# Performance work log

Hardware: AMD Instinct MI355X
Metric: run time of the kernel (lower is better)

## Reference

```python
import jax, jax.numpy as jnp
import numpy as np

B, D, NQ, NS = 64, 64, 2048, 2048

def setup_inputs() -> dict:
    key = jax.random.key(0)
    k1, k2 = jax.random.split(key)
    query_local = jax.random.normal(k1, (B, D, NQ), dtype=jnp.float32)
    support_local = jax.random.normal(k2, (B, D, NS), dtype=jnp.float32)
    return {"query_local": query_local, "support_local": support_local}

def reference(query_local, support_local):
    # sim[b, q, s] = sum_d query[b, d, q] * support[b, d, s]  -> (B, N_q, N_s)
    sim = jnp.einsum('bdq,bds->bqs', query_local, support_local)
    best_sim = jnp.max(sim, axis=2)        # (B, N_q)
    return jnp.mean(best_sim, axis=1)      # (B,)
```

## Files before the change

### kernel.cpp

```cpp
#include <hip/hip_runtime.h>
#include <hip/hip_bf16.h>

#define NB 64
#define ND 64
#define NQ 2048
#define NS 2048
#define QBLK 512
#define SBLK 64
#define QPB 4
#define NSPLIT 2
#define NSS (NS / NSPLIT)
#define NT (NSS / SBLK)

typedef float f32x4 __attribute__((ext_vector_type(4)));
typedef short bf16x8 __attribute__((ext_vector_type(8)));
typedef int i32x4 __attribute__((ext_vector_type(4)));

__device__ inline i32x4 pack8(const float* f) {
  union { __hip_bfloat162 h2[4]; i32x4 v; } u;
  #pragma unroll
  for (int p = 0; p < 4; ++p)
    u.h2[p] = __float22bfloat162_rn(float2{f[2 * p], f[2 * p + 1]});
  return u.v;
}

#define BAR() asm volatile("s_waitcnt lgkmcnt(0)\n\ts_barrier" ::: "memory")

__global__ __launch_bounds__(512, 2) void bmd_main(
    const float* __restrict__ Q, const float* __restrict__ S,
    float* __restrict__ part) {
  const int bid = blockIdx.x;
  const int b  = bid & (NB - 1);
  const int qb = (bid >> 6) & (QPB - 1);
  const int ss = bid >> 8;
  const int q0 = qb * QBLK;
  const int sbase = ss * NSS;
  const int tid = threadIdx.x;
  const int lane = tid & 63;
  const int w = tid >> 6;

  __shared__ char sT[2][SBLK * 128];

  const float* Qb = Q + (size_t)b * ND * NQ;
  const float* Sb = S + (size_t)b * ND * NS;

  const int dbq = (tid >> 3) & 7;
  const int sl = (tid & 7) + ((tid >> 6) << 3);
  const int byt = sl * 128 + ((dbq ^ (sl & 7)) << 4);
  const float* stage_src = Sb + (size_t)dbq * 8 * NS + sbase;

  float fA[8], fB[8];
  {
    const float* s0 = stage_src + sl;
    #pragma unroll
    for (int e = 0; e < 8; ++e) fA[e] = s0[(size_t)e * NS];
    const float* s1 = stage_src + SBLK + sl;
    #pragma unroll
    for (int e = 0; e < 8; ++e) fB[e] = s1[(size_t)e * NS];
  }

  i32x4 afrag[4][2];
  {
    const int qrow = q0 + w * 64 + (lane & 15);
    const int dbase = (lane >> 4) * 8;
    for (int mf = 0; mf < 4; ++mf)
      for (int ks = 0; ks < 2; ++ks) {
        const int d0 = ks * 32 + dbase;
        float f[8];
        #pragma unroll
        for (int e = 0; e < 8; ++e)
          f[e] = Qb[(size_t)(d0 + e) * NQ + (qrow + mf * 16)];
        afrag[mf][ks] = pack8(f);
      }
  }

  const f32x4 kZero = {0.f, 0.f, 0.f, 0.f};
  f32x4 rmax[4];
  #pragma unroll
  for (int mf = 0; mf < 4; ++mf)
    rmax[mf] = f32x4{-INFINITY, -INFINITY, -INFINITY, -INFINITY};

#define COMPUTE(buf)                                                          \
  {                                                                           \
    __builtin_amdgcn_s_setprio(1);                                            \
    _Pragma("unroll")                                                         \
    for (int nfp = 0; nfp < 2; ++nfp) {                                       \
      const int scol0 = nfp * 32 + (lane & 15);                               \
      bf16x8 bfr0[2], bfr1[2];                                                \
      _Pragma("unroll")                                                       \
      for (int ks = 0; ks < 2; ++ks) {                                        \
        const int slot = ((ks * 4 + (lane >> 4)) ^ (scol0 & 7)) << 4;         \
        bfr0[ks] = *reinterpret_cast<const bf16x8*>((buf) + scol0 * 128 + slot);        \
        bfr1[ks] = *reinterpret_cast<const bf16x8*>((buf) + (scol0 + 16) * 128 + slot); \
      }                                                                       \
      _Pragma("unroll")                                                       \
      for (int mf = 0; mf < 4; ++mf) {                                        \
        const bf16x8 a0 = __builtin_bit_cast(bf16x8, afrag[mf][0]);           \
        const bf16x8 a1 = __builtin_bit_cast(bf16x8, afrag[mf][1]);           \
        f32x4 acc0 = __builtin_amdgcn_mfma_f32_16x16x32_bf16(a0, bfr0[0], kZero, 0, 0, 0); \
        f32x4 acc1 = __builtin_amdgcn_mfma_f32_16x16x32_bf16(a0, bfr1[0], kZero, 0, 0, 0); \
        acc0 = __builtin_amdgcn_mfma_f32_16x16x32_bf16(a1, bfr0[1], acc0, 0, 0, 0);        \
        acc1 = __builtin_amdgcn_mfma_f32_16x16x32_bf16(a1, bfr1[1], acc1, 0, 0, 0);        \
        _Pragma("unroll")                                                     \
        for (int j = 0; j < 4; ++j)                                           \
          rmax[mf][j] = fmaxf(rmax[mf][j], fmaxf(acc0[j], acc1[j]));          \
      }                                                                       \
    }                                                                         \
    __builtin_amdgcn_s_setprio(0);                                            \
  }

  *reinterpret_cast<i32x4*>(sT[0] + byt) = pack8(fA);
  BAR();

  for (int i = 0; i < NT / 2; ++i) {
    const int t = 2 * i;
    if (t + 2 < NT) {
      const float* src = stage_src + (t + 2) * SBLK + sl;
      #pragma unroll
      for (int e = 0; e < 8; ++e) fA[e] = src[(size_t)e * NS];
    }
    *reinterpret_cast<i32x4*>(sT[1] + byt) = pack8(fB);
    COMPUTE(sT[0]);
    BAR();
    if (t + 3 < NT) {
      const float* src = stage_src + (t + 3) * SBLK + sl;
      #pragma unroll
      for (int e = 0; e < 8; ++e) fB[e] = src[(size_t)e * NS];
    }
    if (t + 2 < NT)
      *reinterpret_cast<i32x4*>(sT[0] + byt) = pack8(fA);
    COMPUTE(sT[1]);
    BAR();
  }
#undef COMPUTE

  float* rowp = part + (size_t)bid * QBLK + w * 64;
  #pragma unroll
  for (int mf = 0; mf < 4; ++mf) {
    #pragma unroll
    for (int j = 0; j < 4; ++j) {
      float v = rmax[mf][j];
      v = fmaxf(v, __shfl_xor(v, 1));
      v = fmaxf(v, __shfl_xor(v, 2));
      v = fmaxf(v, __shfl_xor(v, 4));
      v = fmaxf(v, __shfl_xor(v, 8));
      if ((lane & 15) == 0)
        rowp[mf * 16 + (lane >> 4) * 4 + j] = v;
    }
  }
}

__global__ void bmd_reduce(const float* __restrict__ part, float* __restrict__ out) {
  const int b = blockIdx.x;
  const int tid = threadIdx.x;
  __shared__ float ws4[4];
  float sum = 0.f;
  #pragma unroll
  for (int k = 0; k < NQ / 256; ++k) {
    const int q = k * 256 + tid;
    const int qb = q >> 9;
    const int row = q & (QBLK - 1);
    float m = -INFINITY;
    #pragma unroll
    for (int ssi = 0; ssi < NSPLIT; ++ssi)
      m = fmaxf(m, part[((size_t)((ssi * QPB + qb) * NB + b)) * QBLK + row]);
    sum += m;
  }
  #pragma unroll
  for (int o = 1; o < 64; o <<= 1) sum += __shfl_xor(sum, o);
  if ((tid & 63) == 0) ws4[tid >> 6] = sum;
  __syncthreads();
  if (tid == 0) out[b] = (ws4[0] + ws4[1] + ws4[2] + ws4[3]) * (1.0f / NQ);
}

extern "C" void kernel_launch(void* const* d_in, const int* in_sizes, int n_in,
                              void* d_out, int out_size, void* d_ws, size_t ws_size,
                              hipStream_t stream) {
  const float* Q = (const float*)d_in[0];
  const float* S = (const float*)d_in[1];
  float* out = (float*)d_out;
  float* part = (float*)d_ws;
  bmd_main<<<dim3(NB * QPB * NSPLIT), dim3(512), 0, stream>>>(Q, S, part);
  bmd_reduce<<<dim3(NB), dim3(256), 0, stream>>>(part, out);
}
```

Before: 51.54 us.

## Split tile compute into barrier-separated phases interleaving LDS loads, staging and MFMA

Each 64-column tile computation is split into two half-phases. Every phase issues its LDS fragment reads first, then the global load or LDS store for the next tile, then a barrier before the MFMA block. The aim is to spread global and LDS traffic across the whole iteration and overlap it with matrix work across waves, similar to a ping-pong schedule. In exchange the loop runs about four times as many s_barrier instructions, which adds synchronization stalls. Correctness depends on waitcnt placement relative to those barriers.

```diff
diff --git a/kernel.cpp b/kernel.cpp
--- a/kernel.cpp
+++ b/kernel.cpp
@@ -24,8 +24,6 @@
   return u.v;
 }
 
-#define BAR() asm volatile("s_waitcnt lgkmcnt(0)\n\ts_barrier" ::: "memory")
-
 __global__ __launch_bounds__(512, 2) void bmd_main(
     const float* __restrict__ Q, const float* __restrict__ S,
     float* __restrict__ part) {
@@ -40,6 +38,8 @@
   const int w = tid >> 6;
 
   __shared__ char sT[2][SBLK * 128];
+  char* const sT0p = sT[0];
+  char* const sT1p = sT[1];
 
   const float* Qb = Q + (size_t)b * ND * NQ;
   const float* Sb = S + (size_t)b * ND * NS;
@@ -80,59 +80,64 @@
   for (int mf = 0; mf < 4; ++mf)
     rmax[mf] = f32x4{-INFINITY, -INFINITY, -INFINITY, -INFINITY};
 
-#define COMPUTE(buf)                                                          \
+#define PHASE(bufptr, nfp, STAGE_CODE)                                        \
   {                                                                           \
+    const int scol0 = (nfp) * 32 + (lane & 15);                               \
+    bf16x8 bfr0[2], bfr1[2];                                                  \
+    _Pragma("unroll")                                                         \
+    for (int ks = 0; ks < 2; ++ks) {                                          \
+      const int slot = ((ks * 4 + (lane >> 4)) ^ (scol0 & 7)) << 4;           \
+      bfr0[ks] = *reinterpret_cast<const bf16x8*>((bufptr) + scol0 * 128 + slot);        \
+      bfr1[ks] = *reinterpret_cast<const bf16x8*>((bufptr) + (scol0 + 16) * 128 + slot); \
+    }                                                                         \
+    STAGE_CODE;                                                               \
+    asm volatile("s_barrier" ::: "memory");                                   \
+    asm volatile("s_waitcnt lgkmcnt(0)" ::: "memory");                        \
     __builtin_amdgcn_s_setprio(1);                                            \
     _Pragma("unroll")                                                         \
-    for (int nfp = 0; nfp < 2; ++nfp) {                                       \
-      const int scol0 = nfp * 32 + (lane & 15);                               \
-      bf16x8 bfr0[2], bfr1[2];                                                \
+    for (int mf = 0; mf < 4; ++mf) {                                          \
+      const bf16x8 a0 = __builtin_bit_cast(bf16x8, afrag[mf][0]);             \
+      const bf16x8 a1 = __builtin_bit_cast(bf16x8, afrag[mf][1]);             \
+      f32x4 acc0 = __builtin_amdgcn_mfma_f32_16x16x32_bf16(a0, bfr0[0], kZero, 0, 0, 0); \
+      f32x4 acc1 = __builtin_amdgcn_mfma_f32_16x16x32_bf16(a0, bfr1[0], kZero, 0, 0, 0); \
+      acc0 = __builtin_amdgcn_mfma_f32_16x16x32_bf16(a1, bfr0[1], acc0, 0, 0, 0);        \
+      acc1 = __builtin_amdgcn_mfma_f32_16x16x32_bf16(a1, bfr1[1], acc1, 0, 0, 0);        \
       _Pragma("unroll")                                                       \
-      for (int ks = 0; ks < 2; ++ks) {                                        \
-        const int slot = ((ks * 4 + (lane >> 4)) ^ (scol0 & 7)) << 4;         \
-        bfr0[ks] = *reinterpret_cast<const bf16x8*>((buf) + scol0 * 128 + slot);        \
-        bfr1[ks] = *reinterpret_cast<const bf16x8*>((buf) + (scol0 + 16) * 128 + slot); \
-      }                                                                       \
-      _Pragma("unroll")                                                       \
-      for (int mf = 0; mf < 4; ++mf) {                                        \
-        const bf16x8 a0 = __builtin_bit_cast(bf16x8, afrag[mf][0]);           \
-        const bf16x8 a1 = __builtin_bit_cast(bf16x8, afrag[mf][1]);           \
-        f32x4 acc0 = __builtin_amdgcn_mfma_f32_16x16x32_bf16(a0, bfr0[0], kZero, 0, 0, 0); \
-        f32x4 acc1 = __builtin_amdgcn_mfma_f32_16x16x32_bf16(a0, bfr1[0], kZero, 0, 0, 0); \
-        acc0 = __builtin_amdgcn_mfma_f32_16x16x32_bf16(a1, bfr0[1], acc0, 0, 0, 0);        \
-        acc1 = __builtin_amdgcn_mfma_f32_16x16x32_bf16(a1, bfr1[1], acc1, 0, 0, 0);        \
-        _Pragma("unroll")                                                     \
-        for (int j = 0; j < 4; ++j)                                           \
-          rmax[mf][j] = fmaxf(rmax[mf][j], fmaxf(acc0[j], acc1[j]));          \
-      }                                                                       \
+      for (int j = 0; j < 4; ++j)                                             \
+        rmax[mf][j] = fmaxf(rmax[mf][j], fmaxf(acc0[j], acc1[j]));            \
     }                                                                         \
     __builtin_amdgcn_s_setprio(0);                                            \
+    asm volatile("s_barrier" ::: "memory");                                   \
   }
 
-  *reinterpret_cast<i32x4*>(sT[0] + byt) = pack8(fA);
-  BAR();
+  *reinterpret_cast<i32x4*>(sT0p + byt) = pack8(fA);
+  asm volatile("s_waitcnt lgkmcnt(0)\n\ts_barrier" ::: "memory");
 
   for (int i = 0; i < NT / 2; ++i) {
     const int t = 2 * i;
-    if (t + 2 < NT) {
-      const float* src = stage_src + (t + 2) * SBLK + sl;
-      #pragma unroll
-      for (int e = 0; e < 8; ++e) fA[e] = src[(size_t)e * NS];
-    }
-    *reinterpret_cast<i32x4*>(sT[1] + byt) = pack8(fB);
-    COMPUTE(sT[0]);
-    BAR();
-    if (t + 3 < NT) {
-      const float* src = stage_src + (t + 3) * SBLK + sl;
-      #pragma unroll
-      for (int e = 0; e < 8; ++e) fB[e] = src[(size_t)e * NS];
-    }
-    if (t + 2 < NT)
-      *reinterpret_cast<i32x4*>(sT[0] + byt) = pack8(fA);
-    COMPUTE(sT[1]);
-    BAR();
+    PHASE(sT0p, 0, {
+      if (t + 2 < NT) {
+        const float* src = stage_src + (t + 2) * SBLK + sl;
+        _Pragma("unroll")
+        for (int e = 0; e < 8; ++e) fA[e] = src[(size_t)e * NS];
+      }
+    });
+    PHASE(sT0p, 1, {
+      *reinterpret_cast<i32x4*>(sT1p + byt) = pack8(fB);
+    });
+    PHASE(sT1p, 0, {
+      if (t + 3 < NT) {
+        const float* src = stage_src + (t + 3) * SBLK + sl;
+        _Pragma("unroll")
+        for (int e = 0; e < 8; ++e) fB[e] = src[(size_t)e * NS];
+      }
+    });
+    PHASE(sT1p, 1, {
+      if (t + 2 < NT)
+        *reinterpret_cast<i32x4*>(sT0p + byt) = pack8(fA);
+    });
   }
-#undef COMPUTE
+#undef PHASE
 
   float* rowp = part + (size_t)bid * QBLK + w * 64;
   #pragma unroll
```

After: 53.20 us. 1.03x slower.
